# Optimization experiments

Hardware: AMD Instinct MI355X
Metric: run time of the kernel (lower is better)

Reference implementation:

```python
import jax, jax.numpy as jnp
import numpy as np

D = 768
H = 8
HD = D // H
FF = 4 * D


def _linear_params(key, din, dout):
    kw, kb = jax.random.split(key)
    lim = 1.0 / np.sqrt(din)
    W = jax.random.uniform(kw, (din, dout), jnp.float32, -lim, lim)
    b = jax.random.uniform(kb, (dout,), jnp.float32, -lim, lim)
    return W, b


def setup_inputs() -> dict:
    key = jax.random.key(0)
    ks = jax.random.split(key, 8)
    x = jax.random.normal(ks[0], (16, 1024, D), jnp.float32)
    Wq, bq = _linear_params(ks[1], D, D)
    Wk, bk = _linear_params(ks[2], D, D)
    Wv, bv = _linear_params(ks[3], D, D)
    Wo, bo = _linear_params(ks[4], D, D)
    W1, b1 = _linear_params(ks[5], D, FF)
    W2, b2 = _linear_params(ks[6], FF, D)
    gamma = jnp.ones((D,), jnp.float32)
    beta = jnp.zeros((D,), jnp.float32)
    return {"x": x, "gamma": gamma, "beta": beta,
            "Wq": Wq, "bq": bq, "Wk": Wk, "bk": bk, "Wv": Wv, "bv": bv,
            "Wo": Wo, "bo": bo, "W1": W1, "b1": b1, "W2": W2, "b2": b2}


def _layernorm(x, gamma, beta, eps=1e-5):
    mu = jnp.mean(x, axis=-1, keepdims=True)
    var = jnp.var(x, axis=-1, keepdims=True)
    return (x - mu) * jax.lax.rsqrt(var + eps) * gamma + beta


def _block(x, gamma, beta, Wq, bq, Wk, bk, Wv, bv, Wo, bo, W1, b1, W2, b2):
    b, n, d = x.shape
    residual = x
    h = _layernorm(x, gamma, beta)
    # QKV projections -> [b, h, n, hd]
    q = (h @ Wq + bq).reshape(b, n, H, HD).transpose(0, 2, 1, 3)
    k = (h @ Wk + bk).reshape(b, n, H, HD).transpose(0, 2, 1, 3)
    v = (h @ Wv + bv).reshape(b, n, H, HD).transpose(0, 2, 1, 3)
    scale = HD ** 0.5
    scores = jnp.einsum('bhid,bhjd->bhij', q, k) / scale
    attn = jax.nn.softmax(scores, axis=-1)
    out = jnp.einsum('bhij,bhjd->bhid', attn, v)
    out = out.transpose(0, 2, 1, 3).reshape(b, n, d)
    out = out @ Wo + bo
    out = out + residual
    residual = out
    h = _layernorm(out, gamma, beta)  # same LN params reused (as in source)
    h = jax.nn.gelu(h @ W1 + b1, approximate=False)
    h = h @ W2 + b2
    return h + residual


def reference(x, gamma, beta, Wq, bq, Wk, bk, Wv, bv, Wo, bo, W1, b1, W2, b2):
    return _block(x, gamma, beta, Wq, bq, Wk, bk, Wv, bv, Wo, bo, W1, b1, W2, b2)
```

## Files before the change

### kernel.cpp

```cpp
#include <hip/hip_runtime.h>

typedef unsigned short u16;
typedef float f32x4 __attribute__((ext_vector_type(4)));
typedef __bf16 bf16x8 __attribute__((ext_vector_type(8)));

#define AS1 __attribute__((address_space(1)))
#define AS3 __attribute__((address_space(3)))

__device__ __forceinline__ float bf2f(u16 h) {
  return __uint_as_float(((unsigned)h) << 16);
}
__device__ __forceinline__ u16 f2bf(float f) {
  unsigned u = __float_as_uint(f);
  unsigned r = (u + 0x7FFFu + ((u >> 16) & 1u)) >> 16;
  return (u16)r;
}
__device__ __forceinline__ void gload16(const u16* g, u16* l) {
  __builtin_amdgcn_global_load_lds((const AS1 void*)g, (AS3 void*)l, 16, 0, 0);
}

__global__ void transpose_k(const float* __restrict__ in, u16* __restrict__ out,
                            int R, int C) {
  __shared__ u16 t[32][33];
  int c0 = blockIdx.x * 32, r0 = blockIdx.y * 32;
  int tx = threadIdx.x & 31, ty = threadIdx.x >> 5;
  for (int i = 0; i < 32; i += 8)
    t[ty + i][tx] = f2bf(in[(size_t)(r0 + ty + i) * C + c0 + tx]);
  __syncthreads();
  for (int i = 0; i < 32; i += 8)
    out[(size_t)(c0 + ty + i) * R + r0 + tx] = t[tx][ty + i];
}

__global__ void vtrans_k(const u16* __restrict__ v, u16* __restrict__ vt) {
  __shared__ u16 t[32][33];
  int bh = blockIdx.z, b = bh >> 3, h = bh & 7;
  int n0 = blockIdx.y * 32, d0 = blockIdx.x * 32;
  int tx = threadIdx.x & 31, ty = threadIdx.x >> 5;
  const u16* src = v + (size_t)(b * 1024) * 768 + h * 96;
  for (int i = 0; i < 32; i += 8)
    t[ty + i][tx] = src[(size_t)(n0 + ty + i) * 768 + d0 + tx];
  __syncthreads();
  u16* dst = vt + ((size_t)bh * 96 + d0) * 1024 + n0;
  for (int i = 0; i < 32; i += 8)
    dst[(size_t)(ty + i) * 1024 + tx] = t[tx][ty + i];
}

__global__ __launch_bounds__(256) void ln_f32_k(const float* __restrict__ x,
                                                const float* __restrict__ gamma,
                                                const float* __restrict__ beta,
                                                u16* __restrict__ out) {
  __shared__ float red[8];
  int row = blockIdx.x, t = threadIdx.x;
  const float* xr = x + (size_t)row * 768;
  float v[3], s = 0.f, s2 = 0.f;
#pragma unroll
  for (int i = 0; i < 3; i++) {
    v[i] = xr[t + i * 256];
    s += v[i]; s2 += v[i] * v[i];
  }
#pragma unroll
  for (int off = 1; off < 64; off <<= 1) {
    s += __shfl_xor(s, off, 64);
    s2 += __shfl_xor(s2, off, 64);
  }
  int w = t >> 6;
  if ((t & 63) == 0) { red[w] = s; red[4 + w] = s2; }
  __syncthreads();
  s = red[0] + red[1] + red[2] + red[3];
  s2 = red[4] + red[5] + red[6] + red[7];
  float mu = s * (1.f / 768.f);
  float var = s2 * (1.f / 768.f) - mu * mu;
  float rs = rsqrtf(var + 1e-5f);
  u16* orow = out + (size_t)row * 768;
#pragma unroll
  for (int i = 0; i < 3; i++) {
    int c = t + i * 256;
    orow[c] = f2bf((v[i] - mu) * rs * gamma[c] + beta[c]);
  }
}

#define BM 128
#define BN 128
#define BK 32

template <int EPI>
__global__ __launch_bounds__(256, 4) void gemm_bt(
    const u16* __restrict__ A, const u16* __restrict__ Bt,
    const float* __restrict__ bias, const float* __restrict__ res,
    void* __restrict__ Cv, int M, int N, int K, int lda) {
  __shared__ u16 As[2][BM * BK];
  __shared__ u16 Bs[2][BN * BK];
  int tid = threadIdx.x, lane = tid & 63, w = tid >> 6;
  int l15 = lane & 15, quad = lane >> 4;
  int wm = (w >> 1) * 64, wn = (w & 1) * 64;
  int GX = gridDim.x;
  int f = blockIdx.y * GX + blockIdx.x;
  int mpx = GX >> 3;
  int xcd = f & 7, idx = f >> 3;
  int m0 = (xcd * mpx + (idx % mpx)) * BM;
  int n0 = (idx / mpx) * BN;
  int NT = K / BK;
#pragma unroll
  for (int i = 0; i < 2; i++) {
    int c = w * 2 + i;
    int r = c * 16 + l15, col = quad * 8;
    gload16(A + (size_t)(m0 + r) * lda + col, As[0] + c * 512);
    gload16(Bt + (size_t)(n0 + r) * K + col, Bs[0] + c * 512);
  }
  f32x4 acc[4][4] = {};
  for (int t = 0; t < NT; t++) {
    int cur = t & 1;
    __builtin_amdgcn_s_barrier();
    int k0 = (t + 1 < NT) ? (t + 1) * BK : 0;
#pragma unroll
    for (int i = 0; i < 2; i++) {
      int c = w * 2 + i;
      int r = c * 16 + l15, col = quad * 8;
      gload16(A + (size_t)(m0 + r) * lda + k0 + col, As[cur ^ 1] + c * 512);
      gload16(Bt + (size_t)(n0 + r) * K + k0 + col, Bs[cur ^ 1] + c * 512);
    }
    asm volatile("s_waitcnt vmcnt(4)" ::: "memory");
    __builtin_amdgcn_s_barrier();
    const u16* ab = As[cur];
    const u16* bb = Bs[cur];
    bf16x8 af[4], bfv[4];
#pragma unroll
    for (int i = 0; i < 4; i++) {
      af[i] = *(const bf16x8*)(ab + ((w >> 1) * 4 + i) * 512 + lane * 8);
      bfv[i] = *(const bf16x8*)(bb + ((w & 1) * 4 + i) * 512 + lane * 8);
    }
#pragma unroll
    for (int mt = 0; mt < 4; mt++)
#pragma unroll
      for (int nt = 0; nt < 4; nt++)
        acc[mt][nt] = __builtin_amdgcn_mfma_f32_16x16x32_bf16(
            af[mt], bfv[nt], acc[mt][nt], 0, 0, 0);
  }
  asm volatile("s_waitcnt vmcnt(0)" ::: "memory");
#pragma unroll
  for (int nt = 0; nt < 4; nt++) {
    int col = n0 + wn + nt * 16 + l15;
    float bv = bias[col];
#pragma unroll
    for (int mt = 0; mt < 4; mt++) {
      int row = m0 + wm + mt * 16 + quad * 4;
#pragma unroll
      for (int r = 0; r < 4; r++) {
        float v = acc[mt][nt][r] + bv;
        size_t idx2 = (size_t)(row + r) * N + col;
        if (EPI == 4) {
          v += res[idx2];
          ((float*)Cv)[idx2] = v;
        } else {
          if (EPI == 2) v = 0.5f * v * (1.0f + erff(v * 0.70710678118654752f));
          ((u16*)Cv)[idx2] = f2bf(v);
        }
      }
    }
  }
}

#define QSS 104
#define VSS 72
#define PSS 72
__global__ __launch_bounds__(256, 2) void attn_k(const u16* __restrict__ q,
                                                 const u16* __restrict__ k,
                                                 const u16* __restrict__ vt,
                                                 u16* __restrict__ o) {
  __shared__ u16 qs[64 * QSS];
  __shared__ u16 ks[2][64 * QSS];
  __shared__ u16 vts[2][96 * VSS];
  __shared__ u16 ps[4 * 16 * PSS];
  int tid = threadIdx.x, lane = tid & 63, w = tid >> 6;
  int l15 = lane & 15, quad = lane >> 4;
  int f = blockIdx.y * 16 + blockIdx.x;
  int xcd = f & 7, idx = f >> 3;
  int bh = xcd * 16 + (idx & 15);
  int qt = idx >> 4;
  int b = bh >> 3, h = bh & 7;
  const u16* qbase = q + (size_t)(b * 1024 + qt * 64) * 768 + h * 96;
  const u16* kbase = k + (size_t)(b * 1024) * 768 + h * 96;
  const u16* vtbase = vt + (size_t)bh * 96 * 1024;
  int kr[3], ko[3], vr[3], vo[3];
#pragma unroll
  for (int i = 0; i < 3; i++) {
    int c = tid + i * 256;
    kr[i] = c / 12; ko[i] = (c % 12) * 8;
    vr[i] = c >> 3; vo[i] = (c & 7) * 8;
  }
#pragma unroll
  for (int i = 0; i < 3; i++)
    *(uint4*)(qs + kr[i] * QSS + ko[i]) =
        *(const uint4*)(qbase + (size_t)kr[i] * 768 + ko[i]);
  uint4 kreg[3], vreg[3];
#pragma unroll
  for (int i = 0; i < 3; i++) {
    kreg[i] = *(const uint4*)(kbase + (size_t)kr[i] * 768 + ko[i]);
    vreg[i] = *(const uint4*)(vtbase + (size_t)vr[i] * 1024 + vo[i]);
  }
#pragma unroll
  for (int i = 0; i < 3; i++) {
    *(uint4*)(ks[0] + kr[i] * QSS + ko[i]) = kreg[i];
    *(uint4*)(vts[0] + vr[i] * VSS + vo[i]) = vreg[i];
  }
  __syncthreads();

  float mi[4], li[4];
#pragma unroll
  for (int r = 0; r < 4; r++) { mi[r] = -1e30f; li[r] = 0.f; }
  f32x4 oacc[6] = {};
  const float scale = 0.10206207261596577f;
  for (int kt = 0; kt < 16; kt++) {
    int cur = kt & 1, nxt = cur ^ 1;
    int ktn = (kt + 1) & 15;
#pragma unroll
    for (int i = 0; i < 3; i++) {
      kreg[i] = *(const uint4*)(kbase + (size_t)(ktn * 64 + kr[i]) * 768 + ko[i]);
      vreg[i] = *(const uint4*)(vtbase + (size_t)vr[i] * 1024 + ktn * 64 + vo[i]);
    }
    f32x4 s[4] = {};
#pragma unroll
    for (int kk = 0; kk < 3; kk++) {
      bf16x8 a = *(const bf16x8*)(qs + (w * 16 + l15) * QSS + kk * 32 + quad * 8);
#pragma unroll
      for (int nt = 0; nt < 4; nt++) {
        bf16x8 bb =
            *(const bf16x8*)(ks[cur] + (nt * 16 + l15) * QSS + kk * 32 + quad * 8);
        s[nt] = __builtin_amdgcn_mfma_f32_16x16x32_bf16(a, bb, s[nt], 0, 0, 0);
      }
    }
#pragma unroll
    for (int r = 0; r < 4; r++) {
      float sv[4], mx = -1e30f;
#pragma unroll
      for (int nt = 0; nt < 4; nt++) {
        sv[nt] = s[nt][r];
        mx = fmaxf(mx, sv[nt]);
      }
#pragma unroll
      for (int off = 1; off < 16; off <<= 1) mx = fmaxf(mx, __shfl_xor(mx, off, 16));
      float mnew = fmaxf(mi[r], mx);
      float alpha = __expf((mi[r] - mnew) * scale);
      float rs = 0.f;
#pragma unroll
      for (int nt = 0; nt < 4; nt++) {
        sv[nt] = __expf((sv[nt] - mnew) * scale);
        rs += sv[nt];
      }
      li[r] = li[r] * alpha + rs;
      mi[r] = mnew;
#pragma unroll
      for (int ht = 0; ht < 6; ht++) oacc[ht][r] *= alpha;
      int prow = quad * 4 + r;
#pragma unroll
      for (int nt = 0; nt < 4; nt++)
        ps[w * 16 * PSS + prow * PSS + nt * 16 + l15] = f2bf(sv[nt]);
    }
    asm volatile("s_waitcnt lgkmcnt(0)" ::: "memory");
#pragma unroll
    for (int kk = 0; kk < 2; kk++) {
      bf16x8 a = *(const bf16x8*)(ps + w * 16 * PSS + l15 * PSS + kk * 32 + quad * 8);
#pragma unroll
      for (int ht = 0; ht < 6; ht++) {
        bf16x8 bb =
            *(const bf16x8*)(vts[cur] + (ht * 16 + l15) * VSS + kk * 32 + quad * 8);
        oacc[ht] = __builtin_amdgcn_mfma_f32_16x16x32_bf16(a, bb, oacc[ht], 0, 0, 0);
      }
    }
#pragma unroll
    for (int i = 0; i < 3; i++) {
      *(uint4*)(ks[nxt] + kr[i] * QSS + ko[i]) = kreg[i];
      *(uint4*)(vts[nxt] + vr[i] * VSS + vo[i]) = vreg[i];
    }
    __syncthreads();
  }
#pragma unroll
  for (int r = 0; r < 4; r++)
#pragma unroll
    for (int off = 1; off < 16; off <<= 1) li[r] += __shfl_xor(li[r], off, 16);
  u16* obase = o + (size_t)(b * 1024 + qt * 64 + w * 16) * 768 + h * 96;
#pragma unroll
  for (int r = 0; r < 4; r++) {
    float inv = 1.0f / li[r];
    int row = quad * 4 + r;
#pragma unroll
    for (int ht = 0; ht < 6; ht++)
      obase[(size_t)row * 768 + ht * 16 + l15] = f2bf(oacc[ht][r] * inv);
  }
}

extern "C" void kernel_launch(void* const* d_in, const int* in_sizes, int n_in,
                              void* d_out, int out_size, void* d_ws,
                              size_t ws_size, hipStream_t stream) {
  const float* x = (const float*)d_in[0];
  const float* gamma = (const float*)d_in[1];
  const float* beta = (const float*)d_in[2];
  const float* Wq = (const float*)d_in[3];
  const float* bq = (const float*)d_in[4];
  const float* Wk = (const float*)d_in[5];
  const float* bk = (const float*)d_in[6];
  const float* Wv = (const float*)d_in[7];
  const float* bv = (const float*)d_in[8];
  const float* Wo = (const float*)d_in[9];
  const float* bo = (const float*)d_in[10];
  const float* W1 = (const float*)d_in[11];
  const float* b1 = (const float*)d_in[12];
  const float* W2 = (const float*)d_in[13];
  const float* b2 = (const float*)d_in[14];
  float* out = (float*)d_out;

  char* ws = (char*)d_ws;
  size_t off = 0;
  auto alloc = [&](size_t elems) {
    u16* p = (u16*)(ws + off);
    off += elems * sizeof(u16);
    return p;
  };
  u16* WqT = alloc(768 * 768);
  u16* WkT = alloc(768 * 768);
  u16* WvT = alloc(768 * 768);
  u16* WoT = alloc(768 * 768);
  u16* W1T = alloc((size_t)768 * 3072);
  u16* W2T = alloc((size_t)3072 * 768);
  u16* hb = alloc((size_t)16384 * 768);
  u16* qb = alloc((size_t)16384 * 768);
  u16* kb = alloc((size_t)16384 * 768);
  u16* vb = alloc((size_t)16384 * 768);

  transpose_k<<<dim3(24, 24), 256, 0, stream>>>(Wq, WqT, 768, 768);
  transpose_k<<<dim3(24, 24), 256, 0, stream>>>(Wk, WkT, 768, 768);
  transpose_k<<<dim3(24, 24), 256, 0, stream>>>(Wv, WvT, 768, 768);
  transpose_k<<<dim3(24, 24), 256, 0, stream>>>(Wo, WoT, 768, 768);
  transpose_k<<<dim3(96, 24), 256, 0, stream>>>(W1, W1T, 768, 3072);
  transpose_k<<<dim3(24, 96), 256, 0, stream>>>(W2, W2T, 3072, 768);

  ln_f32_k<<<16384, 256, 0, stream>>>(x, gamma, beta, hb);
  gemm_bt<0><<<dim3(128, 6), 256, 0, stream>>>(hb, WqT, bq, nullptr, qb,
                                               16384, 768, 768, 768);
  gemm_bt<0><<<dim3(128, 6), 256, 0, stream>>>(hb, WkT, bk, nullptr, kb,
                                               16384, 768, 768, 768);
  gemm_bt<0><<<dim3(128, 6), 256, 0, stream>>>(hb, WvT, bv, nullptr, vb,
                                               16384, 768, 768, 768);
  vtrans_k<<<dim3(3, 32, 128), 256, 0, stream>>>(vb, hb);
  attn_k<<<dim3(16, 128), 256, 0, stream>>>(qb, kb, hb, vb);
  gemm_bt<4><<<dim3(128, 6), 256, 0, stream>>>(vb, WoT, bo, x, out,
                                               16384, 768, 768, 768);
  ln_f32_k<<<16384, 256, 0, stream>>>(out, gamma, beta, kb);
  u16* fbuf = hb;
  for (int c = 0; c < 2; c++) {
    const u16* h2c = kb + (size_t)c * 8192 * 768;
    const float* y1c = out + (size_t)c * 8192 * 768;
    float* outc = out + (size_t)c * 8192 * 768;
    gemm_bt<2><<<dim3(64, 24), 256, 0, stream>>>(h2c, W1T, b1, nullptr, fbuf,
                                                 8192, 3072, 768, 768);
    gemm_bt<4><<<dim3(64, 6), 256, 0, stream>>>(fbuf, W2T, b2, y1c, outc,
                                                8192, 768, 3072, 3072);
  }
}
```

Before: 864.2 us.

## Fuse QKV projections into one GEMM and triple-buffer GEMM LDS pipeline

Runs the Q, K and V projections as a single GEMM with N=2304 over contiguous transposed weights and a packed bias, writing an interleaved QKV buffer that attention and the V transpose read with a larger stride. The four square weight transposes become one batched launch. The GEMM moves from double to triple LDS buffering with a prefetch distance of two tiles and occupancy hint lowered from 4 to 3. It also reuses the output buffer as V-transpose scratch. The goal is fewer launches, more reuse of A tiles, and better latency hiding, at the cost of extra LDS and less occupancy.

```diff
diff --git a/kernel.cpp b/kernel.cpp
--- a/kernel.cpp
+++ b/kernel.cpp
@@ -31,14 +31,40 @@
     out[(size_t)(c0 + ty + i) * R + r0 + tx] = t[tx][ty + i];
 }
 
-__global__ void vtrans_k(const u16* __restrict__ v, u16* __restrict__ vt) {
+__global__ void transpose4_k(const float* __restrict__ s0, const float* __restrict__ s1,
+                             const float* __restrict__ s2, const float* __restrict__ s3,
+                             u16* __restrict__ d0, u16* __restrict__ d1,
+                             u16* __restrict__ d2, u16* __restrict__ d3) {
+  __shared__ u16 t[32][33];
+  const float* in = (blockIdx.z == 0) ? s0 : (blockIdx.z == 1) ? s1
+                    : (blockIdx.z == 2) ? s2 : s3;
+  u16* out = (blockIdx.z == 0) ? d0 : (blockIdx.z == 1) ? d1
+             : (blockIdx.z == 2) ? d2 : d3;
+  int c0 = blockIdx.x * 32, r0 = blockIdx.y * 32;
+  int tx = threadIdx.x & 31, ty = threadIdx.x >> 5;
+  for (int i = 0; i < 32; i += 8)
+    t[ty + i][tx] = f2bf(in[(size_t)(r0 + ty + i) * 768 + c0 + tx]);
+  __syncthreads();
+  for (int i = 0; i < 32; i += 8)
+    out[(size_t)(c0 + ty + i) * 768 + r0 + tx] = t[tx][ty + i];
+}
+
+__global__ void pack3_k(const float* __restrict__ a, const float* __restrict__ b,
+                        const float* __restrict__ c, float* __restrict__ out) {
+  int i = blockIdx.x * 256 + threadIdx.x;
+  float v = (i < 768) ? a[i] : (i < 1536) ? b[i - 768] : c[i - 1536];
+  out[i] = v;
+}
+
+#define QLD 2304
+__global__ void vtrans_k(const u16* __restrict__ qkv, u16* __restrict__ vt) {
   __shared__ u16 t[32][33];
   int bh = blockIdx.z, b = bh >> 3, h = bh & 7;
   int n0 = blockIdx.y * 32, d0 = blockIdx.x * 32;
   int tx = threadIdx.x & 31, ty = threadIdx.x >> 5;
-  const u16* src = v + (size_t)(b * 1024) * 768 + h * 96;
-  for (int i = 0; i < 32; i += 8)
-    t[ty + i][tx] = src[(size_t)(n0 + ty + i) * 768 + d0 + tx];
+  const u16* src = qkv + (size_t)(b * 1024) * QLD + 1536 + h * 96;
+  for (int i = 0; i < 32; i += 8)
+    t[ty + i][tx] = src[(size_t)(n0 + ty + i) * QLD + d0 + tx];
   __syncthreads();
   u16* dst = vt + ((size_t)bh * 96 + d0) * 1024 + n0;
   for (int i = 0; i < 32; i += 8)
@@ -84,12 +110,12 @@
 #define BK 32
 
 template <int EPI>
-__global__ __launch_bounds__(256, 4) void gemm_bt(
+__global__ __launch_bounds__(256, 3) void gemm_bt(
     const u16* __restrict__ A, const u16* __restrict__ Bt,
     const float* __restrict__ bias, const float* __restrict__ res,
     void* __restrict__ Cv, int M, int N, int K, int lda) {
-  __shared__ u16 As[2][BM * BK];
-  __shared__ u16 Bs[2][BN * BK];
+  __shared__ u16 As[3][BM * BK];
+  __shared__ u16 Bs[3][BN * BK];
   int tid = threadIdx.x, lane = tid & 63, w = tid >> 6;
   int l15 = lane & 15, quad = lane >> 4;
   int wm = (w >> 1) * 64, wn = (w & 1) * 64;
@@ -101,25 +127,28 @@
   int n0 = (idx / mpx) * BN;
   int NT = K / BK;
 #pragma unroll
-  for (int i = 0; i < 2; i++) {
-    int c = w * 2 + i;
-    int r = c * 16 + l15, col = quad * 8;
-    gload16(A + (size_t)(m0 + r) * lda + col, As[0] + c * 512);
-    gload16(Bt + (size_t)(n0 + r) * K + col, Bs[0] + c * 512);
+  for (int pt = 0; pt < 2; pt++) {
+#pragma unroll
+    for (int i = 0; i < 2; i++) {
+      int c = w * 2 + i;
+      int r = c * 16 + l15, col = pt * BK + quad * 8;
+      gload16(A + (size_t)(m0 + r) * lda + col, As[pt] + c * 512);
+      gload16(Bt + (size_t)(n0 + r) * K + col, Bs[pt] + c * 512);
+    }
   }
   f32x4 acc[4][4] = {};
   for (int t = 0; t < NT; t++) {
-    int cur = t & 1;
+    int cur = t % 3, nx = (t + 2) % 3;
     __builtin_amdgcn_s_barrier();
-    int k0 = (t + 1 < NT) ? (t + 1) * BK : 0;
+    int k0 = (t + 2 < NT) ? (t + 2) * BK : 0;
 #pragma unroll
     for (int i = 0; i < 2; i++) {
       int c = w * 2 + i;
       int r = c * 16 + l15, col = quad * 8;
-      gload16(A + (size_t)(m0 + r) * lda + k0 + col, As[cur ^ 1] + c * 512);
-      gload16(Bt + (size_t)(n0 + r) * K + k0 + col, Bs[cur ^ 1] + c * 512);
-    }
-    asm volatile("s_waitcnt vmcnt(4)" ::: "memory");
+      gload16(A + (size_t)(m0 + r) * lda + k0 + col, As[nx] + c * 512);
+      gload16(Bt + (size_t)(n0 + r) * K + k0 + col, Bs[nx] + c * 512);
+    }
+    asm volatile("s_waitcnt vmcnt(8)" ::: "memory");
     __builtin_amdgcn_s_barrier();
     const u16* ab = As[cur];
     const u16* bb = Bs[cur];
@@ -163,8 +192,7 @@
 #define QSS 104
 #define VSS 72
 #define PSS 72
-__global__ __launch_bounds__(256, 2) void attn_k(const u16* __restrict__ q,
-                                                 const u16* __restrict__ k,
+__global__ __launch_bounds__(256, 2) void attn_k(const u16* __restrict__ qkv,
                                                  const u16* __restrict__ vt,
                                                  u16* __restrict__ o) {
   __shared__ u16 qs[64 * QSS];
@@ -178,8 +206,8 @@
   int bh = xcd * 16 + (idx & 15);
   int qt = idx >> 4;
   int b = bh >> 3, h = bh & 7;
-  const u16* qbase = q + (size_t)(b * 1024 + qt * 64) * 768 + h * 96;
-  const u16* kbase = k + (size_t)(b * 1024) * 768 + h * 96;
+  const u16* qbase = qkv + (size_t)(b * 1024 + qt * 64) * QLD + h * 96;
+  const u16* kbase = qkv + (size_t)(b * 1024) * QLD + 768 + h * 96;
   const u16* vtbase = vt + (size_t)bh * 96 * 1024;
   int kr[3], ko[3], vr[3], vo[3];
 #pragma unroll
@@ -191,11 +219,11 @@
 #pragma unroll
   for (int i = 0; i < 3; i++)
     *(uint4*)(qs + kr[i] * QSS + ko[i]) =
-        *(const uint4*)(qbase + (size_t)kr[i] * 768 + ko[i]);
+        *(const uint4*)(qbase + (size_t)kr[i] * QLD + ko[i]);
   uint4 kreg[3], vreg[3];
 #pragma unroll
   for (int i = 0; i < 3; i++) {
-    kreg[i] = *(const uint4*)(kbase + (size_t)kr[i] * 768 + ko[i]);
+    kreg[i] = *(const uint4*)(kbase + (size_t)kr[i] * QLD + ko[i]);
     vreg[i] = *(const uint4*)(vtbase + (size_t)vr[i] * 1024 + vo[i]);
   }
 #pragma unroll
@@ -215,7 +243,7 @@
     int ktn = (kt + 1) & 15;
 #pragma unroll
     for (int i = 0; i < 3; i++) {
-      kreg[i] = *(const uint4*)(kbase + (size_t)(ktn * 64 + kr[i]) * 768 + ko[i]);
+      kreg[i] = *(const uint4*)(kbase + (size_t)(ktn * 64 + kr[i]) * QLD + ko[i]);
       vreg[i] = *(const uint4*)(vtbase + (size_t)vr[i] * 1024 + ktn * 64 + vo[i]);
     }
     f32x4 s[4] = {};
@@ -322,38 +350,32 @@
   u16* WoT = alloc(768 * 768);
   u16* W1T = alloc((size_t)768 * 3072);
   u16* W2T = alloc((size_t)3072 * 768);
+  float* bqkv = (float*)(ws + off); off += 2304 * sizeof(float);
   u16* hb = alloc((size_t)16384 * 768);
-  u16* qb = alloc((size_t)16384 * 768);
-  u16* kb = alloc((size_t)16384 * 768);
-  u16* vb = alloc((size_t)16384 * 768);
-
-  transpose_k<<<dim3(24, 24), 256, 0, stream>>>(Wq, WqT, 768, 768);
-  transpose_k<<<dim3(24, 24), 256, 0, stream>>>(Wk, WkT, 768, 768);
-  transpose_k<<<dim3(24, 24), 256, 0, stream>>>(Wv, WvT, 768, 768);
-  transpose_k<<<dim3(24, 24), 256, 0, stream>>>(Wo, WoT, 768, 768);
+  u16* qkvb = alloc((size_t)16384 * 2304);
+  u16* vtb = (u16*)d_out;
+
+  transpose4_k<<<dim3(24, 24, 4), 256, 0, stream>>>(Wq, Wk, Wv, Wo,
+                                                    WqT, WkT, WvT, WoT);
   transpose_k<<<dim3(96, 24), 256, 0, stream>>>(W1, W1T, 768, 3072);
   transpose_k<<<dim3(24, 96), 256, 0, stream>>>(W2, W2T, 3072, 768);
+  pack3_k<<<9, 256, 0, stream>>>(bq, bk, bv, bqkv);
 
   ln_f32_k<<<16384, 256, 0, stream>>>(x, gamma, beta, hb);
-  gemm_bt<0><<<dim3(128, 6), 256, 0, stream>>>(hb, WqT, bq, nullptr, qb,
+  gemm_bt<0><<<dim3(128, 18), 256, 0, stream>>>(hb, WqT, bqkv, nullptr, qkvb,
+                                                16384, 2304, 768, 768);
+  vtrans_k<<<dim3(3, 32, 128), 256, 0, stream>>>(qkvb, vtb);
+  attn_k<<<dim3(16, 128), 256, 0, stream>>>(qkvb, vtb, hb);
+  gemm_bt<4><<<dim3(128, 6), 256, 0, stream>>>(hb, WoT, bo, x, out,
                                                16384, 768, 768, 768);
-  gemm_bt<0><<<dim3(128, 6), 256, 0, stream>>>(hb, WkT, bk, nullptr, kb,
-                                               16384, 768, 768, 768);
-  gemm_bt<0><<<dim3(128, 6), 256, 0, stream>>>(hb, WvT, bv, nullptr, vb,
-                                               16384, 768, 768, 768);
-  vtrans_k<<<dim3(3, 32, 128), 256, 0, stream>>>(vb, hb);
-  attn_k<<<dim3(16, 128), 256, 0, stream>>>(qb, kb, hb, vb);
-  gemm_bt<4><<<dim3(128, 6), 256, 0, stream>>>(vb, WoT, bo, x, out,
-                                               16384, 768, 768, 768);
-  ln_f32_k<<<16384, 256, 0, stream>>>(out, gamma, beta, kb);
-  u16* fbuf = hb;
+  ln_f32_k<<<16384, 256, 0, stream>>>(out, gamma, beta, hb);
   for (int c = 0; c < 2; c++) {
-    const u16* h2c = kb + (size_t)c * 8192 * 768;
+    const u16* h2c = hb + (size_t)c * 8192 * 768;
     const float* y1c = out + (size_t)c * 8192 * 768;
     float* outc = out + (size_t)c * 8192 * 768;
-    gemm_bt<2><<<dim3(64, 24), 256, 0, stream>>>(h2c, W1T, b1, nullptr, fbuf,
+    gemm_bt<2><<<dim3(64, 24), 256, 0, stream>>>(h2c, W1T, b1, nullptr, qkvb,
                                                  8192, 3072, 768, 768);
-    gemm_bt<4><<<dim3(64, 6), 256, 0, stream>>>(fbuf, W2T, b2, y1c, outc,
+    gemm_bt<4><<<dim3(64, 6), 256, 0, stream>>>(qkvb, W2T, b2, y1c, outc,
                                                 8192, 768, 3072, 3072);
   }
 }
```

After: 857.8 us. Within noise of the previous version (-0.7%).
